# Optimization experiments

Measured on AMD Instinct MI355X. Metric: run time of the kernel, lower is better.

The kernel has to match this reference:

```python
import jax, jax.numpy as jnp
import numpy as np

B, S, I, C, H, O = 512, 512, 64, 4, 100, 7


def setup_inputs() -> dict:
    key = jax.random.key(0)
    ks = jax.random.split(key, 4)
    w = lambda k, shape: (jax.random.normal(k, shape, jnp.float32) * 0.05)
    return {
        "x": jax.random.normal(ks[0], (B, S, I), jnp.float32),
        "context_inputs": jnp.ones((C,), jnp.float32) / C,
        "Wf_w": w(ks[1], (H, I + C + H)),
        "Wf_b": jnp.zeros((H,), jnp.float32),
        "Wh_w": w(ks[2], (H, I + C + H)),
        "Wh_b": jnp.zeros((H,), jnp.float32),
        "ro_w": w(ks[3], (O, H)),
        "ro_b": jnp.zeros((O,), jnp.float32),
    }


def reference(x, context_inputs, Wf_w, Wf_b, Wh_w, Wh_b, ro_w, ro_b):
    b, s, i = x.shape
    c = context_inputs.shape[0]
    h_dim = Wf_w.shape[0]
    ic = i + c
    # concatenate the learned context to every timestep (concatenate_context=True path)
    xc = jnp.concatenate([x, jnp.broadcast_to(context_inputs, (b, s, c))], axis=2)
    # split weights into input-driven and hidden-driven parts
    Wf_x, Wf_h = Wf_w[:, :ic], Wf_w[:, ic:]
    Wh_x, Wh_h = Wh_w[:, :ic], Wh_w[:, ic:]
    # precompute all input projections (large GEMMs outside the scan)
    xf = jnp.einsum("bsi,hi->bsh", xc, Wf_x) + Wf_b  # forget-gate input term
    xh = jnp.einsum("bsi,hi->bsh", xc, Wh_x) + Wh_b  # candidate input term

    def step(h, inp):
        xf_t, xh_t = inp  # each (b, h_dim)
        f = jax.nn.sigmoid(xf_t + h @ Wf_h.T)
        h_tilde = jnp.tanh(xh_t + (f * h) @ Wh_h.T)
        h_new = (1.0 - f) * h + f * h_tilde
        return h_new, h_new

    h0 = jnp.zeros((b, h_dim), x.dtype)
    _, hs = jax.lax.scan(step, h0, (xf.transpose(1, 0, 2), xh.transpose(1, 0, 2)))
    hidden_states = hs.transpose(1, 0, 2)  # (b, s, h_dim)
    last_hidden = hidden_states[:, -1, :]
    output = last_hidden @ ro_w.T + ro_b  # (b, O)
    return output, hidden_states
```

## Files before the change

### kernel.cpp

```cpp
#include <hip/hip_runtime.h>

typedef _Float16 half2_t __attribute__((ext_vector_type(2)));

#define NB 512
#define NS 512
#define NI 64
#define NH 100
#define NO 7
#define WROW 168

__device__ __forceinline__ float dot2f(half2_t a, half2_t b, float c) {
    return __builtin_amdgcn_fdot2(a, b, c, false);
}
__device__ __forceinline__ half2_t pack2(float a, float b) {
    half2_t r; r[0] = (_Float16)a; r[1] = (_Float16)b; return r;
}
__device__ __forceinline__ unsigned pack2u(float a, float b) {
    return __builtin_bit_cast(unsigned, pack2(a, b));
}
__device__ __forceinline__ half2_t h2(unsigned u) {
    return __builtin_bit_cast(half2_t, u);
}

__global__ __launch_bounds__(64, 1) void agent_scan(
    const float* __restrict__ x,
    const float* __restrict__ ctx,
    const float* __restrict__ Wf_w,
    const float* __restrict__ Wf_b,
    const float* __restrict__ Wh_w,
    const float* __restrict__ Wh_b,
    const float* __restrict__ ro_w,
    const float* __restrict__ ro_b,
    float* __restrict__ out)
{
    const int b = blockIdx.x, lane = threadIdx.x;
    const int j0 = 2 * lane;
    const bool act = (lane < NH / 2);

    __shared__ __align__(16) unsigned vx[32];
    __shared__ __align__(16) unsigned vh[52];
    __shared__ __align__(16) unsigned vg[52];
    __shared__ __align__(16) float hfin[NH];

    if (lane < 52) { vh[lane] = 0u; vg[lane] = 0u; }

    const float s = act ? 1.f : 0.f;
    const int jc0 = act ? j0 : 0;
    half2_t wfx[2][32], whx[2][32], wfh[2][50], whh[2][50];
    float cf[2], ch[2];
    const float c0 = ctx[0], c1 = ctx[1], c2 = ctx[2], c3 = ctx[3];
    #pragma unroll
    for (int o = 0; o < 2; ++o) {
        const float* rf = Wf_w + (size_t)(jc0 + o) * WROW;
        const float* rh = Wh_w + (size_t)(jc0 + o) * WROW;
        #pragma unroll
        for (int u = 0; u < 16; ++u) {
            const float4 a  = *(const float4*)(rf + 4 * u);
            const float4 bb = *(const float4*)(rh + 4 * u);
            wfx[o][2*u]   = pack2(s * a.x,  s * a.y);
            wfx[o][2*u+1] = pack2(s * a.z,  s * a.w);
            whx[o][2*u]   = pack2(s * bb.x, s * bb.y);
            whx[o][2*u+1] = pack2(s * bb.z, s * bb.w);
        }
        #pragma unroll
        for (int u = 0; u < 25; ++u) {
            const float4 a  = *(const float4*)(rf + 68 + 4 * u);
            const float4 bb = *(const float4*)(rh + 68 + 4 * u);
            wfh[o][2*u]   = pack2(s * a.x,  s * a.y);
            wfh[o][2*u+1] = pack2(s * a.z,  s * a.w);
            whh[o][2*u]   = pack2(s * bb.x, s * bb.y);
            whh[o][2*u+1] = pack2(s * bb.z, s * bb.w);
        }
        const float4 cfv = *(const float4*)(rf + 64);
        const float4 chv = *(const float4*)(rh + 64);
        cf[o] = Wf_b[jc0+o] + cfv.x*c0 + cfv.y*c1 + cfv.z*c2 + cfv.w*c3;
        ch[o] = Wh_b[jc0+o] + chv.x*c0 + chv.y*c1 + chv.z*c2 + chv.w*c3;
    }

    const float* xrow = x + (size_t)b * NS * NI;
    float4 xp = make_float4(0.f, 0.f, 0.f, 0.f);
    if (lane < 16) {
        const float4 v = *(const float4*)(xrow + 4 * lane);
        *(uint2*)&vx[2*lane] = make_uint2(pack2u(v.x, v.y), pack2u(v.z, v.w));
        xp = *(const float4*)(xrow + NI + 4 * lane);
    }
    asm volatile("" ::: "memory");

    float* hidbase = out + NB * NO + (size_t)b * NS * NH;
    float h0 = 0.f, h1 = 0.f;

    for (int t = 0; t < NS; ++t) {
        half2_t xb[32];
        #pragma unroll
        for (int r = 0; r < 8; ++r) {
            const uint4 v = *(const uint4*)&vx[4*r];
            xb[4*r] = h2(v.x); xb[4*r+1] = h2(v.y); xb[4*r+2] = h2(v.z); xb[4*r+3] = h2(v.w);
        }
        half2_t hb[52];
        #pragma unroll
        for (int r = 0; r < 13; ++r) {
            const uint4 v = *(const uint4*)&vh[4*r];
            hb[4*r] = h2(v.x); hb[4*r+1] = h2(v.y); hb[4*r+2] = h2(v.z); hb[4*r+3] = h2(v.w);
        }
        asm volatile("" ::: "memory");
        if (lane < 16)
            *(uint2*)&vx[2*lane] = make_uint2(pack2u(xp.x, xp.y), pack2u(xp.z, xp.w));
        {
            const int tn = (t + 2 < NS) ? t + 2 : NS - 1;
            if (lane < 16) xp = *(const float4*)(xrow + (size_t)tn * NI + 4 * lane);
        }

        float af0=0.f, af1=0.f, ag0=0.f, ag1=0.f;
        float ah0=0.f, ah1=0.f, ai0=0.f, ai1=0.f;
        #pragma unroll
        for (int u = 0; u < 32; u += 2) {
            af0 = dot2f(wfx[0][u],   xb[u],   af0);
            af1 = dot2f(wfx[0][u+1], xb[u+1], af1);
            ag0 = dot2f(wfx[1][u],   xb[u],   ag0);
            ag1 = dot2f(wfx[1][u+1], xb[u+1], ag1);
            ah0 = dot2f(whx[0][u],   xb[u],   ah0);
            ah1 = dot2f(whx[0][u+1], xb[u+1], ah1);
            ai0 = dot2f(whx[1][u],   xb[u],   ai0);
            ai1 = dot2f(whx[1][u+1], xb[u+1], ai1);
        }
        float bf0=0.f, bf1=0.f, bg0=0.f, bg1=0.f;
        #pragma unroll
        for (int u = 0; u < 50; u += 2) {
            bf0 = dot2f(wfh[0][u],   hb[u],   bf0);
            bf1 = dot2f(wfh[0][u+1], hb[u+1], bf1);
            bg0 = dot2f(wfh[1][u],   hb[u],   bg0);
            bg1 = dot2f(wfh[1][u+1], hb[u+1], bg1);
        }
        const float zf0 = cf[0] + af0 + af1 + bf0 + bf1;
        const float zf1 = cf[1] + ag0 + ag1 + bg0 + bg1;
        const float f0 = __fdividef(1.f, 1.f + __expf(-zf0));
        const float f1 = __fdividef(1.f, 1.f + __expf(-zf1));

        if (act) vg[lane] = pack2u(f0 * h0, f1 * h1);
        asm volatile("" ::: "memory");

        half2_t gb[52];
        #pragma unroll
        for (int r = 0; r < 13; ++r) {
            const uint4 v = *(const uint4*)&vg[4*r];
            gb[4*r] = h2(v.x); gb[4*r+1] = h2(v.y); gb[4*r+2] = h2(v.z); gb[4*r+3] = h2(v.w);
        }
        float bh0=0.f, bh1=0.f, bi0=0.f, bi1=0.f;
        #pragma unroll
        for (int u = 0; u < 50; u += 2) {
            bh0 = dot2f(whh[0][u],   gb[u],   bh0);
            bh1 = dot2f(whh[0][u+1], gb[u+1], bh1);
            bi0 = dot2f(whh[1][u],   gb[u],   bi0);
            bi1 = dot2f(whh[1][u+1], gb[u+1], bi1);
        }
        const float zh0 = ch[0] + ah0 + ah1 + bh0 + bh1;
        const float zh1 = ch[1] + ai0 + ai1 + bi0 + bi1;
        const float e0 = __expf(2.f * zh0), e1 = __expf(2.f * zh1);
        const float th0 = 1.f - __fdividef(2.f, e0 + 1.f);
        const float th1 = 1.f - __fdividef(2.f, e1 + 1.f);
        h0 += f0 * (th0 - h0);
        h1 += f1 * (th1 - h1);

        if (act) {
            vh[lane] = pack2u(h0, h1);
            *(float2*)(hidbase + (size_t)t * NH + j0) = make_float2(h0, h1);
        }
        asm volatile("" ::: "memory");
    }

    if (act) *(float2*)&hfin[j0] = make_float2(h0, h1);
    asm volatile("" ::: "memory");
    if (lane < NO) {
        float acc = ro_b[lane];
        const float* rr = ro_w + lane * NH;
        #pragma unroll
        for (int u = 0; u < 25; ++u) {
            const float4 v = *(const float4*)(rr + 4 * u);
            acc += v.x * hfin[4*u] + v.y * hfin[4*u+1] + v.z * hfin[4*u+2] + v.w * hfin[4*u+3];
        }
        out[b * NO + lane] = acc;
    }
}

extern "C" void kernel_launch(void* const* d_in, const int* in_sizes, int n_in,
                              void* d_out, int out_size, void* d_ws, size_t ws_size,
                              hipStream_t stream) {
    const float* x    = (const float*)d_in[0];
    const float* ctx  = (const float*)d_in[1];
    const float* Wf_w = (const float*)d_in[2];
    const float* Wf_b = (const float*)d_in[3];
    const float* Wh_w = (const float*)d_in[4];
    const float* Wh_b = (const float*)d_in[5];
    const float* ro_w = (const float*)d_in[6];
    const float* ro_b = (const float*)d_in[7];
    (void)in_sizes; (void)n_in; (void)out_size; (void)d_ws; (void)ws_size;
    agent_scan<<<dim3(NB), dim3(64), 0, stream>>>(x, ctx, Wf_w, Wf_b, Wh_w, Wh_b, ro_w, ro_b, (float*)d_out);
}
```

Baseline: 880.3 us.

## Precompute input projections in parallel GEMM and split recurrent dots across lanes

Adds a separate kernel that computes the input-driven gate projections for all timesteps at once and stores them as fp16 in the hidden-state output region as scratch. The scan kernel then reads these via a small prefetch ring and spreads each hidden dot product over four lanes with DPP reductions, so only the recurrent matvecs stay on the serial path. This shortens the per-step critical path in exchange for an extra memory round-trip and some fp16 rounding of the projected inputs.

```diff
diff --git a/kernel.cpp b/kernel.cpp
--- a/kernel.cpp
+++ b/kernel.cpp
@@ -15,160 +15,214 @@
 __device__ __forceinline__ half2_t pack2(float a, float b) {
     half2_t r; r[0] = (_Float16)a; r[1] = (_Float16)b; return r;
 }
-__device__ __forceinline__ unsigned pack2u(float a, float b) {
-    return __builtin_bit_cast(unsigned, pack2(a, b));
-}
-__device__ __forceinline__ half2_t h2(unsigned u) {
-    return __builtin_bit_cast(half2_t, u);
+__device__ __forceinline__ half2_t h2u(unsigned u) { return __builtin_bit_cast(half2_t, u); }
+__device__ __forceinline__ float f16lo(unsigned u) {
+    return (float)__builtin_bit_cast(_Float16, (unsigned short)(u & 0xffffu));
+}
+__device__ __forceinline__ float f16hi(unsigned u) {
+    return (float)__builtin_bit_cast(_Float16, (unsigned short)(u >> 16));
+}
+__device__ __forceinline__ float qsum4(float v) {
+    int i = __builtin_bit_cast(int, v);
+    int t = __builtin_amdgcn_update_dpp(0, i, 0xB1, 0xF, 0xF, true);
+    v += __builtin_bit_cast(float, t);
+    i = __builtin_bit_cast(int, v);
+    t = __builtin_amdgcn_update_dpp(0, i, 0x4E, 0xF, 0xF, true);
+    v += __builtin_bit_cast(float, t);
+    return v;
+}
+
+__global__ __launch_bounds__(256, 4) void proj_gemm(
+    const float* __restrict__ x, const float* __restrict__ ctx,
+    const float* __restrict__ Wf_w, const float* __restrict__ Wf_b,
+    const float* __restrict__ Wh_w, const float* __restrict__ Wh_b,
+    float* __restrict__ out)
+{
+    __shared__ __align__(16) half2_t wl[200][32];
+    __shared__ float bl[200];
+    const int tid = threadIdx.x;
+
+    for (int idx = tid; idx < 200 * 32; idx += 256) {
+        const int j = idx >> 5, u = idx & 31;
+        const float* W = (j < 100) ? (Wf_w + (size_t)j * WROW)
+                                   : (Wh_w + (size_t)(j - 100) * WROW);
+        wl[j][u] = pack2(W[2 * u], W[2 * u + 1]);
+    }
+    const float c0 = ctx[0], c1 = ctx[1], c2 = ctx[2], c3 = ctx[3];
+    for (int j = tid; j < 200; j += 256) {
+        const float* W; float bb;
+        if (j < 100) { W = Wf_w + (size_t)j * WROW;        bb = Wf_b[j]; }
+        else         { W = Wh_w + (size_t)(j - 100) * WROW; bb = Wh_b[j - 100]; }
+        bl[j] = bb + W[64]*c0 + W[65]*c1 + W[66]*c2 + W[67]*c3;
+    }
+    __syncthreads();
+
+    const size_t row = (size_t)blockIdx.x * 256 + tid;
+    const float* xp = x + row * NI;
+    half2_t xr[32];
+    #pragma unroll
+    for (int u = 0; u < 16; ++u) {
+        const float4 v = *(const float4*)(xp + 4 * u);
+        xr[2*u]   = pack2(v.x, v.y);
+        xr[2*u+1] = pack2(v.z, v.w);
+    }
+    unsigned* orow = (unsigned*)((_Float16*)(out + NB * NO) + row * 200);
+    #pragma unroll 1
+    for (int c = 0; c < 25; ++c) {
+        float acc[8];
+        #pragma unroll
+        for (int jj = 0; jj < 8; ++jj) {
+            const int j = 8 * c + jj;
+            float a0 = bl[j], a1 = 0.f;
+            const uint4* wr = (const uint4*)&wl[j][0];
+            #pragma unroll
+            for (int u = 0; u < 8; ++u) {
+                const uint4 wv = wr[u];
+                a0 = dot2f(h2u(wv.x), xr[4*u],   a0);
+                a1 = dot2f(h2u(wv.y), xr[4*u+1], a1);
+                a0 = dot2f(h2u(wv.z), xr[4*u+2], a0);
+                a1 = dot2f(h2u(wv.w), xr[4*u+3], a1);
+            }
+            acc[jj] = a0 + a1;
+        }
+        uint4 st;
+        st.x = __builtin_bit_cast(unsigned, pack2(acc[0], acc[1]));
+        st.y = __builtin_bit_cast(unsigned, pack2(acc[2], acc[3]));
+        st.z = __builtin_bit_cast(unsigned, pack2(acc[4], acc[5]));
+        st.w = __builtin_bit_cast(unsigned, pack2(acc[6], acc[7]));
+        *(uint4*)&orow[4 * c] = st;
+    }
 }
 
 __global__ __launch_bounds__(64, 1) void agent_scan(
-    const float* __restrict__ x,
-    const float* __restrict__ ctx,
-    const float* __restrict__ Wf_w,
-    const float* __restrict__ Wf_b,
-    const float* __restrict__ Wh_w,
-    const float* __restrict__ Wh_b,
-    const float* __restrict__ ro_w,
-    const float* __restrict__ ro_b,
+    const float* __restrict__ Wf_w, const float* __restrict__ Wh_w,
+    const float* __restrict__ ro_w, const float* __restrict__ ro_b,
     float* __restrict__ out)
 {
     const int b = blockIdx.x, lane = threadIdx.x;
-    const int j0 = 2 * lane;
-    const bool act = (lane < NH / 2);
-
-    __shared__ __align__(16) unsigned vx[32];
-    __shared__ __align__(16) unsigned vh[52];
-    __shared__ __align__(16) unsigned vg[52];
-    __shared__ __align__(16) float hfin[NH];
-
-    if (lane < 52) { vh[lane] = 0u; vg[lane] = 0u; }
-
-    const float s = act ? 1.f : 0.f;
-    const int jc0 = act ? j0 : 0;
-    half2_t wfx[2][32], whx[2][32], wfh[2][50], whh[2][50];
-    float cf[2], ch[2];
-    const float c0 = ctx[0], c1 = ctx[1], c2 = ctx[2], c3 = ctx[3];
+    const int g = lane >> 2, q = lane & 3;
+
+    __shared__ __align__(16) _Float16 vh[128];
+    __shared__ __align__(16) _Float16 vg[128];
+    __shared__ float hfin[NH];
+
+    ((unsigned*)vh)[lane] = 0u;
+    ((unsigned*)vg)[lane] = 0u;
+
+    half2_t wf[7][13], wh[7][13];
     #pragma unroll
-    for (int o = 0; o < 2; ++o) {
-        const float* rf = Wf_w + (size_t)(jc0 + o) * WROW;
-        const float* rh = Wh_w + (size_t)(jc0 + o) * WROW;
-        #pragma unroll
-        for (int u = 0; u < 16; ++u) {
-            const float4 a  = *(const float4*)(rf + 4 * u);
-            const float4 bb = *(const float4*)(rh + 4 * u);
-            wfx[o][2*u]   = pack2(s * a.x,  s * a.y);
-            wfx[o][2*u+1] = pack2(s * a.z,  s * a.w);
-            whx[o][2*u]   = pack2(s * bb.x, s * bb.y);
-            whx[o][2*u+1] = pack2(s * bb.z, s * bb.w);
-        }
-        #pragma unroll
-        for (int u = 0; u < 25; ++u) {
-            const float4 a  = *(const float4*)(rf + 68 + 4 * u);
-            const float4 bb = *(const float4*)(rh + 68 + 4 * u);
-            wfh[o][2*u]   = pack2(s * a.x,  s * a.y);
-            wfh[o][2*u+1] = pack2(s * a.z,  s * a.w);
-            whh[o][2*u]   = pack2(s * bb.x, s * bb.y);
-            whh[o][2*u+1] = pack2(s * bb.z, s * bb.w);
-        }
-        const float4 cfv = *(const float4*)(rf + 64);
-        const float4 chv = *(const float4*)(rh + 64);
-        cf[o] = Wf_b[jc0+o] + cfv.x*c0 + cfv.y*c1 + cfv.z*c2 + cfv.w*c3;
-        ch[o] = Wh_b[jc0+o] + chv.x*c0 + chv.y*c1 + chv.z*c2 + chv.w*c3;
-    }
-
-    const float* xrow = x + (size_t)b * NS * NI;
-    float4 xp = make_float4(0.f, 0.f, 0.f, 0.f);
-    if (lane < 16) {
-        const float4 v = *(const float4*)(xrow + 4 * lane);
-        *(uint2*)&vx[2*lane] = make_uint2(pack2u(v.x, v.y), pack2u(v.z, v.w));
-        xp = *(const float4*)(xrow + NI + 4 * lane);
-    }
+    for (int o = 0; o < 7; ++o) {
+        const int j = g + 16 * o;
+        const bool valid = (j < NH);
+        const float* rf = Wf_w + (size_t)(valid ? j : 0) * WROW + 68;
+        const float* rh = Wh_w + (size_t)(valid ? j : 0) * WROW + 68;
+        #pragma unroll
+        for (int u = 0; u < 13; ++u) {
+            const int k0 = 26 * q + 2 * u, k1 = k0 + 1;
+            const float f0 = (valid && k0 < NH) ? rf[k0] : 0.f;
+            const float f1 = (valid && k1 < NH) ? rf[k1] : 0.f;
+            const float g0 = (valid && k0 < NH) ? rh[k0] : 0.f;
+            const float g1 = (valid && k1 < NH) ? rh[k1] : 0.f;
+            wf[o][u] = pack2(f0, f1);
+            wh[o][u] = pack2(g0, g1);
+        }
+    }
+
+    const int jA = g + 16 * q;
+    const int jB = g + 16 * (q + 4);
+    const bool hasB = (q <= 2) && (jB < NH);
+    const int jBc = hasB ? jB : 0;
+    const int posA = 32 * (jA / 26) + jA % 26;
+    const int posB = 32 * (jBc / 26) + jBc % 26;
+
+    const unsigned short* xq = (const unsigned short*)(out + NB * NO) + (size_t)b * NS * 200;
+    float* hid = out + NB * NO + (size_t)b * NS * NH;
+
+    unsigned ringA[4], ringB[4];
+    #pragma unroll
+    for (int d = 0; d < 4; ++d) {
+        const size_t ro = (size_t)d * 200;
+        ringA[d] = (unsigned)xq[ro + jA]  | ((unsigned)xq[ro + 100 + jA]  << 16);
+        ringB[d] = (unsigned)xq[ro + jBc] | ((unsigned)xq[ro + 100 + jBc] << 16);
+    }
+
+    float hA = 0.f, hB = 0.f;
     asm volatile("" ::: "memory");
 
-    float* hidbase = out + NB * NO + (size_t)b * NS * NH;
-    float h0 = 0.f, h1 = 0.f;
-
-    for (int t = 0; t < NS; ++t) {
-        half2_t xb[32];
-        #pragma unroll
-        for (int r = 0; r < 8; ++r) {
-            const uint4 v = *(const uint4*)&vx[4*r];
-            xb[4*r] = h2(v.x); xb[4*r+1] = h2(v.y); xb[4*r+2] = h2(v.z); xb[4*r+3] = h2(v.w);
-        }
-        half2_t hb[52];
-        #pragma unroll
-        for (int r = 0; r < 13; ++r) {
-            const uint4 v = *(const uint4*)&vh[4*r];
-            hb[4*r] = h2(v.x); hb[4*r+1] = h2(v.y); hb[4*r+2] = h2(v.z); hb[4*r+3] = h2(v.w);
-        }
+    auto step = [&](int t, int dd) {
+        const uint4 v0 = *(const uint4*)(vh + 32 * q);
+        const uint4 v1 = *(const uint4*)(vh + 32 * q + 8);
+        const uint4 v2 = *(const uint4*)(vh + 32 * q + 16);
+        const unsigned v3 = *(const unsigned*)(vh + 32 * q + 24);
+        half2_t p[13];
+        p[0]=h2u(v0.x); p[1]=h2u(v0.y); p[2]=h2u(v0.z); p[3]=h2u(v0.w);
+        p[4]=h2u(v1.x); p[5]=h2u(v1.y); p[6]=h2u(v1.z); p[7]=h2u(v1.w);
+        p[8]=h2u(v2.x); p[9]=h2u(v2.y); p[10]=h2u(v2.z); p[11]=h2u(v2.w);
+        p[12]=h2u(v3);
+
+        float af[7];
+        #pragma unroll
+        for (int o = 0; o < 7; ++o) {
+            float a = 0.f;
+            #pragma unroll
+            for (int u = 0; u < 13; ++u) a = dot2f(wf[o][u], p[u], a);
+            af[o] = qsum4(a);
+        }
+        const float zA = (q == 0) ? af[0] : (q == 1) ? af[1] : (q == 2) ? af[2] : af[3];
+        const float zB = (q == 0) ? af[4] : (q == 1) ? af[5] : af[6];
+        const float fA = __fdividef(1.f, 1.f + __expf(-(zA + f16lo(ringA[dd]))));
+        const float fB = __fdividef(1.f, 1.f + __expf(-(zB + f16lo(ringB[dd]))));
+
+        vg[posA] = (_Float16)(fA * hA);
+        if (hasB) vg[posB] = (_Float16)(fB * hB);
         asm volatile("" ::: "memory");
-        if (lane < 16)
-            *(uint2*)&vx[2*lane] = make_uint2(pack2u(xp.x, xp.y), pack2u(xp.z, xp.w));
-        {
-            const int tn = (t + 2 < NS) ? t + 2 : NS - 1;
-            if (lane < 16) xp = *(const float4*)(xrow + (size_t)tn * NI + 4 * lane);
-        }
-
-        float af0=0.f, af1=0.f, ag0=0.f, ag1=0.f;
-        float ah0=0.f, ah1=0.f, ai0=0.f, ai1=0.f;
-        #pragma unroll
-        for (int u = 0; u < 32; u += 2) {
-            af0 = dot2f(wfx[0][u],   xb[u],   af0);
-            af1 = dot2f(wfx[0][u+1], xb[u+1], af1);
-            ag0 = dot2f(wfx[1][u],   xb[u],   ag0);
-            ag1 = dot2f(wfx[1][u+1], xb[u+1], ag1);
-            ah0 = dot2f(whx[0][u],   xb[u],   ah0);
-            ah1 = dot2f(whx[0][u+1], xb[u+1], ah1);
-            ai0 = dot2f(whx[1][u],   xb[u],   ai0);
-            ai1 = dot2f(whx[1][u+1], xb[u+1], ai1);
-        }
-        float bf0=0.f, bf1=0.f, bg0=0.f, bg1=0.f;
-        #pragma unroll
-        for (int u = 0; u < 50; u += 2) {
-            bf0 = dot2f(wfh[0][u],   hb[u],   bf0);
-            bf1 = dot2f(wfh[0][u+1], hb[u+1], bf1);
-            bg0 = dot2f(wfh[1][u],   hb[u],   bg0);
-            bg1 = dot2f(wfh[1][u+1], hb[u+1], bg1);
-        }
-        const float zf0 = cf[0] + af0 + af1 + bf0 + bf1;
-        const float zf1 = cf[1] + ag0 + ag1 + bg0 + bg1;
-        const float f0 = __fdividef(1.f, 1.f + __expf(-zf0));
-        const float f1 = __fdividef(1.f, 1.f + __expf(-zf1));
-
-        if (act) vg[lane] = pack2u(f0 * h0, f1 * h1);
+
+        const uint4 w0 = *(const uint4*)(vg + 32 * q);
+        const uint4 w1 = *(const uint4*)(vg + 32 * q + 8);
+        const uint4 w2 = *(const uint4*)(vg + 32 * q + 16);
+        const unsigned w3 = *(const unsigned*)(vg + 32 * q + 24);
+        half2_t r[13];
+        r[0]=h2u(w0.x); r[1]=h2u(w0.y); r[2]=h2u(w0.z); r[3]=h2u(w0.w);
+        r[4]=h2u(w1.x); r[5]=h2u(w1.y); r[6]=h2u(w1.z); r[7]=h2u(w1.w);
+        r[8]=h2u(w2.x); r[9]=h2u(w2.y); r[10]=h2u(w2.z); r[11]=h2u(w2.w);
+        r[12]=h2u(w3);
+
+        float ah[7];
+        #pragma unroll
+        for (int o = 0; o < 7; ++o) {
+            float a = 0.f;
+            #pragma unroll
+            for (int u = 0; u < 13; ++u) a = dot2f(wh[o][u], r[u], a);
+            ah[o] = qsum4(a);
+        }
+        const float yA = (q == 0) ? ah[0] : (q == 1) ? ah[1] : (q == 2) ? ah[2] : ah[3];
+        const float yB = (q == 0) ? ah[4] : (q == 1) ? ah[5] : ah[6];
+        const float eA = __expf(2.f * (yA + f16hi(ringA[dd])));
+        const float eB = __expf(2.f * (yB + f16hi(ringB[dd])));
+        const float thA = 1.f - __fdividef(2.f, eA + 1.f);
+        const float thB = 1.f - __fdividef(2.f, eB + 1.f);
+        hA += fA * (thA - hA);
+        hB += fB * (thB - hB);
+
+        vh[posA] = (_Float16)hA;
+        if (hasB) vh[posB] = (_Float16)hB;
+        float* hrow = hid + (size_t)t * NH;
+        hrow[jA] = hA;
+        if (hasB) hrow[jB] = hB;
+
+        const int rr = (t + 4 < NS) ? t + 4 : NS - 1;
+        const size_t ro = (size_t)rr * 200;
+        ringA[dd] = (unsigned)xq[ro + jA]  | ((unsigned)xq[ro + 100 + jA]  << 16);
+        ringB[dd] = (unsigned)xq[ro + jBc] | ((unsigned)xq[ro + 100 + jBc] << 16);
         asm volatile("" ::: "memory");
-
-        half2_t gb[52];
-        #pragma unroll
-        for (int r = 0; r < 13; ++r) {
-            const uint4 v = *(const uint4*)&vg[4*r];
-            gb[4*r] = h2(v.x); gb[4*r+1] = h2(v.y); gb[4*r+2] = h2(v.z); gb[4*r+3] = h2(v.w);
-        }
-        float bh0=0.f, bh1=0.f, bi0=0.f, bi1=0.f;
-        #pragma unroll
-        for (int u = 0; u < 50; u += 2) {
-            bh0 = dot2f(whh[0][u],   gb[u],   bh0);
-            bh1 = dot2f(whh[0][u+1], gb[u+1], bh1);
-            bi0 = dot2f(whh[1][u],   gb[u],   bi0);
-            bi1 = dot2f(whh[1][u+1], gb[u+1], bi1);
-        }
-        const float zh0 = ch[0] + ah0 + ah1 + bh0 + bh1;
-        const float zh1 = ch[1] + ai0 + ai1 + bi0 + bi1;
-        const float e0 = __expf(2.f * zh0), e1 = __expf(2.f * zh1);
-        const float th0 = 1.f - __fdividef(2.f, e0 + 1.f);
-        const float th1 = 1.f - __fdividef(2.f, e1 + 1.f);
-        h0 += f0 * (th0 - h0);
-        h1 += f1 * (th1 - h1);
-
-        if (act) {
-            vh[lane] = pack2u(h0, h1);
-            *(float2*)(hidbase + (size_t)t * NH + j0) = make_float2(h0, h1);
-        }
-        asm volatile("" ::: "memory");
-    }
-
-    if (act) *(float2*)&hfin[j0] = make_float2(h0, h1);
+    };
+
+    for (int tt = 0; tt < NS; tt += 4) {
+        step(tt, 0); step(tt + 1, 1); step(tt + 2, 2); step(tt + 3, 3);
+    }
+
+    hfin[jA] = hA;
+    if (hasB) hfin[jB] = hB;
     asm volatile("" ::: "memory");
     if (lane < NO) {
         float acc = ro_b[lane];
@@ -194,5 +248,8 @@
     const float* ro_w = (const float*)d_in[6];
     const float* ro_b = (const float*)d_in[7];
     (void)in_sizes; (void)n_in; (void)out_size; (void)d_ws; (void)ws_size;
-    agent_scan<<<dim3(NB), dim3(64), 0, stream>>>(x, ctx, Wf_w, Wf_b, Wh_w, Wh_b, ro_w, ro_b, (float*)d_out);
-}
+    float* out = (float*)d_out;
+
+    proj_gemm<<<dim3((NB * NS) / 256), dim3(256), 0, stream>>>(x, ctx, Wf_w, Wf_b, Wh_w, Wh_b, out);
+    agent_scan<<<dim3(NB), dim3(64), 0, stream>>>(Wf_w, Wh_w, ro_w, ro_b, out);
+}
```

After: 767.5 us. -12.8%, faster.
